# Kernel tuning notes

Measured on AMD Instinct MI355X. Metric: run time of the kernel, lower is better.

Reference implementation:

```python
import jax, jax.numpy as jnp
import numpy as np

B, S, H = 2, 2048, 2048
NH, NKV, HD = 16, 4, 128
ROPE_BASE = 10000.0


def rotate_half(x):
    x1, x2 = jnp.split(x, 2, axis=-1)
    return jnp.concatenate((-x2, x1), axis=-1)


def setup_inputs() -> dict:
    key = jax.random.key(0)
    ks = jax.random.split(key, 6)
    hidden_states = jax.random.normal(ks[0], (B, S, H), dtype=jnp.float32)
    # additive causal mask, as used by HF: 0 on allowed, large negative on masked
    causal = jnp.triu(jnp.full((S, S), -1e9, dtype=jnp.float32), k=1)
    attention_mask = jnp.broadcast_to(causal[None, None], (B, 1, S, S))
    position_ids = jnp.broadcast_to(jnp.arange(S, dtype=jnp.int64)[None], (B, S))
    scale = 1.0 / np.sqrt(H)
    Wq = jax.random.normal(ks[1], (NH * HD, H), dtype=jnp.float32) * scale
    Wk = jax.random.normal(ks[2], (NKV * HD, H), dtype=jnp.float32) * scale
    Wv = jax.random.normal(ks[3], (NKV * HD, H), dtype=jnp.float32) * scale
    Wo = jax.random.normal(ks[4], (H, NH * HD), dtype=jnp.float32) * scale
    return {"hidden_states": hidden_states, "attention_mask": attention_mask,
            "position_ids": position_ids, "Wq": Wq, "Wk": Wk, "Wv": Wv, "Wo": Wo}


def reference(hidden_states, attention_mask, position_ids, Wq, Wk, Wv, Wo):
    b, s, _ = hidden_states.shape
    # projections (torch Linear: y = x W^T)
    q = jnp.einsum('bsh,oh->bso', hidden_states, Wq).reshape(b, s, NH, HD).transpose(0, 2, 1, 3)
    k = jnp.einsum('bsh,oh->bso', hidden_states, Wk).reshape(b, s, NKV, HD).transpose(0, 2, 1, 3)
    v = jnp.einsum('bsh,oh->bso', hidden_states, Wv).reshape(b, s, NKV, HD).transpose(0, 2, 1, 3)
    # RoPE
    inv_freq = 1.0 / (ROPE_BASE ** (jnp.arange(0, HD, 2, dtype=jnp.float32) / HD))  # [HD/2]
    freqs = position_ids.astype(jnp.float32)[:, :, None] * inv_freq[None, None, :]  # [B,S,HD/2]
    emb = jnp.concatenate((freqs, freqs), axis=-1)                                  # [B,S,HD]
    cos = jnp.cos(emb)[:, None]  # [B,1,S,HD]
    sin = jnp.sin(emb)[:, None]
    q = q * cos + rotate_half(q) * sin
    k = k * cos + rotate_half(k) * sin
    # GQA repeat (repeat_interleave along head axis)
    n_rep = NH // NKV
    k = jnp.repeat(k, n_rep, axis=1)
    v = jnp.repeat(v, n_rep, axis=1)
    scale = HD ** -0.5
    attn = jnp.einsum('bhqd,bhkd->bhqk', q, k) * scale
    attn = attn + attention_mask
    attn = jax.nn.softmax(attn.astype(jnp.float32), axis=-1).astype(q.dtype)
    out = jnp.einsum('bhqk,bhkd->bhqd', attn, v)            # [B,NH,S,HD]
    out = out.transpose(0, 2, 1, 3).reshape(b, s, NH * HD)  # [B,S,H]
    return jnp.einsum('bso,ho->bsh', out, Wo)
```

## Files before the change

kernel.cpp:

```cpp
#include <hip/hip_runtime.h>


#define B_ 2
#define S_ 2048
#define H_ 2048
#define NH_ 16
#define NKV_ 4
#define HD_ 128
#define QKV_N 3072

typedef unsigned short u16;
typedef unsigned int u32;
typedef unsigned long long u64;
typedef __attribute__((ext_vector_type(8))) short short8;
typedef __attribute__((ext_vector_type(4))) float floatx4;
typedef __attribute__((ext_vector_type(16))) float floatx16;

__device__ __forceinline__ u16 f2bf(float f) {
    union { float f; u32 u; } v; v.f = f;
    u32 u = v.u;
    return (u16)((u + 0x7fffu + ((u >> 16) & 1u)) >> 16);
}
__device__ __forceinline__ float bf2f(u16 h) {
    union { u32 u; float f; } v; v.u = ((u32)h) << 16;
    return v.f;
}
__device__ __forceinline__ void store_out(u16* p, float v)  { *p = f2bf(v); }
__device__ __forceinline__ void store_out(float* p, float v) { *p = v; }

__device__ __forceinline__ void gload_lds16(const void* g, void* l) {
    __builtin_amdgcn_global_load_lds(
        (const __attribute__((address_space(1))) void*)g,
        (__attribute__((address_space(3))) void*)l, 16, 0, 0);
}

__device__ __forceinline__ u32 cvtpk(float lo, float hi) {
    u32 r;
    asm("v_cvt_pk_bf16_f32 %0, %1, %2" : "=v"(r) : "v"(lo), "v"(hi));
    return r;
}

__device__ __forceinline__ void pl32swap(u32& a, u32& b) {
#if __has_builtin(__builtin_amdgcn_permlane32_swap)
    typedef __attribute__((ext_vector_type(2))) int iv2;
    iv2 r = __builtin_amdgcn_permlane32_swap((int)a, (int)b, false, false);
    a = (u32)r[0];
    b = (u32)r[1];
#else
    asm volatile("v_permlane32_swap_b32 %0, %1" : "+v"(a), "+v"(b));
#endif
}

__global__ __launch_bounds__(256) void cast_all(const float* __restrict__ hs,
                                                const float* __restrict__ Wq,
                                                const float* __restrict__ Wk,
                                                const float* __restrict__ Wv,
                                                const float* __restrict__ Wo,
                                                u16* __restrict__ hs_b,
                                                u16* __restrict__ wqkv_b,
                                                u16* __restrict__ wo_b) {
    int q = blockIdx.x * 256 + threadIdx.x;
    const float* src;
    u16* dst;
    if (q < 2097152)      { src = hs; dst = hs_b; }
    else if (q < 3145728) { q -= 2097152; src = Wq; dst = wqkv_b; }
    else if (q < 3407872) { q -= 3145728; src = Wk; dst = wqkv_b + 2048 * 2048; }
    else if (q < 3670016) { q -= 3407872; src = Wv; dst = wqkv_b + 2560 * 2048; }
    else                  { q -= 3670016; src = Wo; dst = wo_b; }
    float4 f = ((const float4*)src)[q];
    u32 lo = ((u32)f2bf(f.y) << 16) | f2bf(f.x);
    u32 hi2 = ((u32)f2bf(f.w) << 16) | f2bf(f.z);
    *(u64*)(dst + (size_t)q * 4) = (u64)lo | ((u64)hi2 << 32);
}

template <typename OutT>
__global__ __launch_bounds__(256) void gemm128(const u16* __restrict__ A,
                                               const u16* __restrict__ Bm,
                                               OutT* __restrict__ C,
                                               int M, int N, int K) {
    __shared__ __align__(16) u16 As[128][32];
    __shared__ __align__(16) u16 Bs[128][32];
    const int tid  = threadIdx.x;
    const int wave = tid >> 6;
    const int lane = tid & 63;
    const int quad = lane >> 4;
    const int l16  = lane & 15;

    const int nbx = gridDim.x, nby = gridDim.y;
    const int total = nbx * nby;
    int n = (int)blockIdx.y * nbx + (int)blockIdx.x;
    if ((total & 7) == 0) {
        int cpx = total >> 3;
        n = (n & 7) * cpx + (n >> 3);
    }
    const int m0 = (n / nbx) * 128;
    const int n0 = (n % nbx) * 128;

    const int wm = (wave >> 1) * 64;
    const int wn = (wave & 1) * 64;
    const int srow = tid >> 2;
    const int scol = (tid & 3) * 8;

    floatx4 acc[4][4] = {};

    for (int k0 = 0; k0 < K; k0 += 32) {
        __syncthreads();
        gload_lds16(A  + (size_t)(m0 + srow) * K + k0 + scol,      &As[srow][scol]);
        gload_lds16(A  + (size_t)(m0 + 64 + srow) * K + k0 + scol, &As[64 + srow][scol]);
        gload_lds16(Bm + (size_t)(n0 + srow) * K + k0 + scol,      &Bs[srow][scol]);
        gload_lds16(Bm + (size_t)(n0 + 64 + srow) * K + k0 + scol, &Bs[64 + srow][scol]);
        __syncthreads();
        short8 af[4], bfv[4];
        for (int i = 0; i < 4; ++i) {
            af[i]  = *(const short8*)&As[wm + i * 16 + l16][quad * 8];
            bfv[i] = *(const short8*)&Bs[wn + i * 16 + l16][quad * 8];
        }
        for (int mi = 0; mi < 4; ++mi)
            for (int ni = 0; ni < 4; ++ni)
                acc[mi][ni] = __builtin_amdgcn_mfma_f32_16x16x32_bf16(
                    af[mi], bfv[ni], acc[mi][ni], 0, 0, 0);
    }
    for (int mi = 0; mi < 4; ++mi)
        for (int ni = 0; ni < 4; ++ni)
            for (int r = 0; r < 4; ++r) {
                int row = m0 + wm + mi * 16 + quad * 4 + r;
                int col = n0 + wn + ni * 16 + l16;
                store_out(C + (size_t)row * N + col, acc[mi][ni][r]);
            }
}

__global__ __launch_bounds__(256) void rope_trans(u16* __restrict__ buf,
                                                  u16* __restrict__ vt) {
    const int bid = blockIdx.x;
    const int tid = threadIdx.x;
    if (bid < 20480) {
        int i = bid * 256 + tid;
        int hofs, nheads;
        float oscale;
        if (i < 4194304) { hofs = 0;    nheads = 16; oscale = 0.08838834764831845f; }
        else             { i -= 4194304; hofs = 2048; nheads = 4;  oscale = 1.0f; }
        int d = i & 63;
        int t = i >> 6;
        int head = t % nheads;
        int row  = t / nheads;
        int s    = row & (S_ - 1);
        size_t base = (size_t)row * QKV_N + hofs + head * HD_;
        float invf = exp2f(-(float)d * (13.28771237954945f / 64.0f));
        float fr = (float)s * invf;
        float sn, cs;
        sincosf(fr, &sn, &cs);
        float x1 = bf2f(buf[base + d]);
        float x2 = bf2f(buf[base + d + 64]);
        buf[base + d]      = f2bf((x1 * cs - x2 * sn) * oscale);
        buf[base + d + 64] = f2bf((x2 * cs + x1 * sn) * oscale);
    } else {
        __shared__ u16 t[32][33];
        const int b2 = bid - 20480;
        const int bx = b2 & 15, by = (b2 >> 4) & 63, bz = b2 >> 10;
        const int tx = tid & 31, ty = tid >> 5;
        const int c0 = bx * 32, s0 = by * 32, b = bz;
        for (int i = 0; i < 4; ++i)
            t[ty + i * 8][tx] =
                buf[((size_t)(b * S_ + s0 + ty + i * 8)) * QKV_N + 2560 + c0 + tx];
        __syncthreads();
        for (int i = 0; i < 4; ++i)
            vt[((size_t)(b * 512 + c0 + ty + i * 8)) * S_ + s0 + tx] = t[tx][ty + i * 8];
    }
}

__global__ __launch_bounds__(256) void flash_attn(const u16* __restrict__ qkv,
                                                  const u16* __restrict__ vtg,
                                                  u16* __restrict__ o) {
    __shared__ __align__(16) u16 KsL[64 * 128];
    __shared__ __align__(16) u16 VtL[128 * 64];

    const int tid  = threadIdx.x;
    const int wave = tid >> 6;
    const int lane = tid & 63;
    const int l31  = lane & 31;
    const int hi   = lane >> 5;
    const int wq   = wave >> 1;
    const int kb   = wave & 1;

    const int bx = (int)blockIdx.x;
    const int by = (int)blockIdx.y;
    const int flip = (by >> 3) & 1;
    const int a4 = bx & 15;
    const int jq = flip ? a4 : (31 - a4);
    const int bh = (by & 7) | (((by >> 4) & 1) << 3) | ((bx >> 4) << 4);
    const int b   = bh >> 4;
    const int h   = bh & 15;
    const int kvh = h >> 2;
    const int q0  = jq * 64;

    const size_t qb = ((size_t)(b * S_ + q0 + wq * 32 + l31)) * QKV_N + h * HD_;
    short8 qf[8];
#pragma unroll
    for (int mf = 0; mf < 8; ++mf)
        qf[mf] = *(const short8*)(qkv + qb + mf * 16 + hi * 8);

    floatx16 o_acc[4] = {};
    float l_loc = 0.f;

    const size_t kbase = (size_t)(b * S_) * QKV_N + 2048 + kvh * HD_;
    const size_t vbase = (size_t)((b * NKV_ + kvh) * HD_) * S_;
    const int krow_l = (lane >> 4);
    const int kslot  = lane & 15;
    const int vrow_l = (lane >> 3);
    const int vslot  = lane & 7;
    int kr_[4], kc_[4], vr_[4], vc_[4];
#pragma unroll
    for (int p = 0; p < 4; ++p) {
        kr_[p] = 16 * wave + 4 * p + krow_l;
        kc_[p] = (kslot ^ (kr_[p] & 7)) * 8;
        vr_[p] = 32 * wave + 8 * p + vrow_l;
        vc_[p] = (vslot ^ (vr_[p] & 7)) * 8;
    }

    const int rk = kb * 32 + l31;
    const int kswz = rk & 7;

    short8 kreg[4], vreg[4];
#pragma unroll
    for (int p = 0; p < 4; ++p) {
        kreg[p] = *(const short8*)(qkv + kbase + (size_t)kr_[p] * QKV_N + kc_[p]);
        vreg[p] = *(const short8*)(vtg + vbase + (size_t)vr_[p] * S_ + vc_[p]);
    }

    for (int kt = 0; kt <= jq; ++kt) {
        __syncthreads();
#pragma unroll
        for (int p = 0; p < 4; ++p) {
            *(short8*)&KsL[(16 * wave + 4 * p) * 128 + lane * 8] = kreg[p];
            *(short8*)&VtL[(32 * wave + 8 * p) * 64 + lane * 8]  = vreg[p];
        }
        __syncthreads();

        if (kt < jq) {
            const size_t ko = kbase + (size_t)((kt + 1) * 64) * QKV_N;
            const size_t vo = vbase + (size_t)((kt + 1) * 64);
#pragma unroll
            for (int p = 0; p < 4; ++p) {
                kreg[p] = *(const short8*)(qkv + ko + (size_t)kr_[p] * QKV_N + kc_[p]);
                vreg[p] = *(const short8*)(vtg + vo + (size_t)vr_[p] * S_ + vc_[p]);
            }
        }

        floatx16 st = {};
#pragma unroll
        for (int mf = 0; mf < 8; ++mf) {
            short8 kf = *(const short8*)&KsL[rk * 128 + (((mf * 2 + hi) ^ kswz) * 8)];
            st = __builtin_amdgcn_mfma_f32_32x32x16_bf16(kf, qf[mf], st, 0, 0, 0);
        }
        if (kt == jq) {
            int qloc = wq * 32 + l31;
#pragma unroll
            for (int r = 0; r < 16; ++r) {
                int krow = kb * 32 + (r & 3) + 8 * (r >> 2) + 4 * hi;
                if (krow > qloc) st[r] = -INFINITY;
            }
        }
        u32 pk[8];
        float ll = 0.f;
#pragma unroll
        for (int i = 0; i < 8; ++i) {
            float e0 = __expf(st[2 * i]);
            float e1 = __expf(st[2 * i + 1]);
            ll += e0 + e1;
            pk[i] = cvtpk(e0, e1);
        }
        l_loc += ll;
        pl32swap(pk[0], pk[2]);
        pl32swap(pk[1], pk[3]);
        pl32swap(pk[4], pk[6]);
        pl32swap(pk[5], pk[7]);
        union { u32 u[4]; short8 s; } c0, c1;
        c0.u[0] = pk[0]; c0.u[1] = pk[1]; c0.u[2] = pk[2]; c0.u[3] = pk[3];
        c1.u[0] = pk[4]; c1.u[1] = pk[5]; c1.u[2] = pk[6]; c1.u[3] = pk[7];
#pragma unroll
        for (int dblk = 0; dblk < 4; ++dblk) {
            int rv = dblk * 32 + l31;
            int sw = rv & 7;
            short8 va = *(const short8*)&VtL[rv * 64 + (((kb * 4 + hi) ^ sw) * 8)];
            o_acc[dblk] = __builtin_amdgcn_mfma_f32_32x32x16_bf16(va, c0.s, o_acc[dblk], 0, 0, 0);
            short8 vb = *(const short8*)&VtL[rv * 64 + (((kb * 4 + 2 + hi) ^ sw) * 8)];
            o_acc[dblk] = __builtin_amdgcn_mfma_f32_32x32x16_bf16(vb, c1.s, o_acc[dblk], 0, 0, 0);
        }
    }

    float lt = l_loc + __shfl_xor(l_loc, 32, 64);
    __syncthreads();
    float* scr = (float*)KsL;
    if (kb == 1) scr[wq * 64 + lane] = lt;
    __syncthreads();
    float linv = 0.f;
    if (kb == 0) linv = 1.0f / (lt + scr[wq * 64 + lane]);

#pragma unroll
    for (int dblk = 0; dblk < 4; ++dblk) {
        __syncthreads();
        if (kb == 1) {
#pragma unroll
            for (int r = 0; r < 16; ++r)
                scr[wq * 1088 + lane * 17 + r] = o_acc[dblk][r];
        }
        __syncthreads();
        if (kb == 0) {
            const int row = q0 + wq * 32 + l31;
#pragma unroll
            for (int rg = 0; rg < 4; ++rg) {
                float v0 = (o_acc[dblk][rg * 4 + 0] + scr[wq * 1088 + lane * 17 + rg * 4 + 0]) * linv;
                float v1 = (o_acc[dblk][rg * 4 + 1] + scr[wq * 1088 + lane * 17 + rg * 4 + 1]) * linv;
                float v2 = (o_acc[dblk][rg * 4 + 2] + scr[wq * 1088 + lane * 17 + rg * 4 + 2]) * linv;
                float v3 = (o_acc[dblk][rg * 4 + 3] + scr[wq * 1088 + lane * 17 + rg * 4 + 3]) * linv;
                u32 wlo = cvtpk(v0, v1);
                u32 whi = cvtpk(v2, v3);
                int col = h * HD_ + dblk * 32 + rg * 8 + 4 * hi;
                u64 pack = (u64)wlo | ((u64)whi << 32);
                *(u64*)(o + ((size_t)(b * S_ + row)) * H_ + col) = pack;
            }
        }
    }
}

extern "C" void kernel_launch(void* const* d_in, const int* in_sizes, int n_in,
                              void* d_out, int out_size, void* d_ws, size_t ws_size,
                              hipStream_t stream) {
    const float* hs = (const float*)d_in[0];
    const float* Wq = (const float*)d_in[3];
    const float* Wk = (const float*)d_in[4];
    const float* Wv = (const float*)d_in[5];
    const float* Wo = (const float*)d_in[6];

    char* ws = (char*)d_ws;
    const size_t MB = 1024 * 1024;
    u16* hs_b   = (u16*)(ws + 0);
    u16* wqkv_b = (u16*)(ws + 16 * MB);
    u16* vt_b   = (u16*)(ws + 16 * MB);
    u16* wo_b   = (u16*)(ws + 28 * MB);
    u16* qkv    = (u16*)(ws + 36 * MB);

    const int M = B_ * S_;

    cast_all<<<18432, 256, 0, stream>>>(hs, Wq, Wk, Wv, Wo, hs_b, wqkv_b, wo_b);

    gemm128<u16><<<dim3(QKV_N / 128, M / 128), 256, 0, stream>>>(
        hs_b, wqkv_b, qkv, M, QKV_N, H_);

    rope_trans<<<22528, 256, 0, stream>>>(qkv, vt_b);

    flash_attn<<<dim3(32, 32), 256, 0, stream>>>(qkv, vt_b, hs_b);

    gemm128<float><<<dim3(H_ / 128, M / 128), 256, 0, stream>>>(
        hs_b, wo_b, (float*)d_out, M, H_, H_);
}
```

Baseline: 332.1 us.

## Double-buffer LDS tiles in bf16 GEMM to overlap loads with MFMA

```diff
diff --git a/kernel.cpp b/kernel.cpp
--- a/kernel.cpp
+++ b/kernel.cpp
@@ -78,8 +78,8 @@
                                                const u16* __restrict__ Bm,
                                                OutT* __restrict__ C,
                                                int M, int N, int K) {
-    __shared__ __align__(16) u16 As[128][32];
-    __shared__ __align__(16) u16 Bs[128][32];
+    __shared__ __align__(16) u16 As[2][128][32];
+    __shared__ __align__(16) u16 Bs[2][128][32];
     const int tid  = threadIdx.x;
     const int wave = tid >> 6;
     const int lane = tid & 63;
@@ -103,23 +103,45 @@
 
     floatx4 acc[4][4] = {};
 
-    for (int k0 = 0; k0 < K; k0 += 32) {
-        __syncthreads();
-        gload_lds16(A  + (size_t)(m0 + srow) * K + k0 + scol,      &As[srow][scol]);
-        gload_lds16(A  + (size_t)(m0 + 64 + srow) * K + k0 + scol, &As[64 + srow][scol]);
-        gload_lds16(Bm + (size_t)(n0 + srow) * K + k0 + scol,      &Bs[srow][scol]);
-        gload_lds16(Bm + (size_t)(n0 + 64 + srow) * K + k0 + scol, &Bs[64 + srow][scol]);
-        __syncthreads();
-        short8 af[4], bfv[4];
-        for (int i = 0; i < 4; ++i) {
-            af[i]  = *(const short8*)&As[wm + i * 16 + l16][quad * 8];
-            bfv[i] = *(const short8*)&Bs[wn + i * 16 + l16][quad * 8];
-        }
-        for (int mi = 0; mi < 4; ++mi)
-            for (int ni = 0; ni < 4; ++ni)
-                acc[mi][ni] = __builtin_amdgcn_mfma_f32_16x16x32_bf16(
-                    af[mi], bfv[ni], acc[mi][ni], 0, 0, 0);
-    }
+    const u16* a0 = A  + (size_t)(m0 + srow) * K + scol;
+    const u16* a1 = A  + (size_t)(m0 + 64 + srow) * K + scol;
+    const u16* b0 = Bm + (size_t)(n0 + srow) * K + scol;
+    const u16* b1 = Bm + (size_t)(n0 + 64 + srow) * K + scol;
+
+#define STAGE(buf, k0)                                            \
+    do {                                                          \
+        gload_lds16(a0 + (k0), &As[buf][srow][scol]);             \
+        gload_lds16(a1 + (k0), &As[buf][64 + srow][scol]);        \
+        gload_lds16(b0 + (k0), &Bs[buf][srow][scol]);             \
+        gload_lds16(b1 + (k0), &Bs[buf][64 + srow][scol]);        \
+    } while (0)
+
+#define COMPUTE(buf)                                                        \
+    do {                                                                    \
+        short8 af[4], bfv[4];                                               \
+        for (int i = 0; i < 4; ++i) {                                       \
+            af[i]  = *(const short8*)&As[buf][wm + i * 16 + l16][quad * 8]; \
+            bfv[i] = *(const short8*)&Bs[buf][wn + i * 16 + l16][quad * 8]; \
+        }                                                                   \
+        for (int mi = 0; mi < 4; ++mi)                                      \
+            for (int ni = 0; ni < 4; ++ni)                                  \
+                acc[mi][ni] = __builtin_amdgcn_mfma_f32_16x16x32_bf16(      \
+                    af[mi], bfv[ni], acc[mi][ni], 0, 0, 0);                 \
+    } while (0)
+
+    STAGE(0, 0);
+    __syncthreads();
+    for (int k0 = 0; k0 < K; k0 += 64) {
+        STAGE(1, k0 + 32);
+        COMPUTE(0);
+        __syncthreads();
+        if (k0 + 64 < K) STAGE(0, k0 + 64);
+        COMPUTE(1);
+        __syncthreads();
+    }
+#undef STAGE
+#undef COMPUTE
+
     for (int mi = 0; mi < 4; ++mi)
         for (int ni = 0; ni < 4; ++ni)
             for (int r = 0; r < 4; ++r) {
```

New measurement: 324.8 us. -2.2%, faster.
